# Kernel optimization log

Measured on AMD Instinct MI355X. Metric: run time of the kernel, lower is better.

Reference implementation:

```python
import jax, jax.numpy as jnp
import numpy as np

ROUTINGS = 3
EPS = 1e-9

def _squash(s):
    # squash along the capsule-vector (last) axis
    sq = jnp.sum(s * s, axis=-1, keepdims=True)
    return s * (sq / (1.0 + sq)) / jnp.sqrt(sq + EPS)

def setup_inputs() -> dict:
    key = jax.random.key(0)
    k1, k2 = jax.random.split(key)
    B, N, D, d = 32, 64, 128, 128  # batch, num_capsule(=input_num_capsule), dim_capsule, input_dim_capsule
    x = jax.random.normal(k1, (B, N, d), dtype=jnp.float32)
    W = jax.random.normal(k2, (1, N, N, D, d), dtype=jnp.float32)
    return {"x": x, "W": W}

def reference(x, W):
    # u[b,j,k,:] = W[0,j,k] @ x[b,j]  (faithful to broadcast matmul, N==I)
    u = jnp.einsum('jkde,bje->bjkd', W[0], x)  # (B,N,N,D)
    b = jnp.zeros_like(u)                      # routing logits carry D axis per source
    v = None
    for i in range(ROUTINGS):
        c = jax.nn.softmax(b, axis=2)
        s = jnp.sum(c * u, axis=1, keepdims=True)  # (B,1,N,D)
        v = _squash(s)
        if i < ROUTINGS - 1:
            b = b + u * v  # (inputs*outputs).sum over trailing singleton dim
    return v[:, 0, :, :, None]  # (B,N,D,1) matching torch outputs.squeeze(1)
```

## Files before the change

kernel.cpp:

```cpp
#include <hip/hip_runtime.h>

#define NB 32
#define NN 64
#define ND 128
#define NE 128
#define NK 64

typedef float  f32x4  __attribute__((ext_vector_type(4)));
typedef short  short8 __attribute__((ext_vector_type(8)));
typedef __bf16 bf16x8 __attribute__((ext_vector_type(8)));

union Frag { bf16x8 h; short8 s; };

static constexpr size_t U_BYTES = (size_t)NB * NN * ND * NK * 2;
static constexpr size_t V_BYTES = (size_t)NB * ND * NK * 4;
static constexpr size_t WS_NEED = U_BYTES + 2 * V_BYTES;

#define GLOAD16(g, l)                                                   \
    __builtin_amdgcn_global_load_lds(                                   \
        (const __attribute__((address_space(1))) void*)(g),             \
        (__attribute__((address_space(3))) void*)(l), 16, 0, 0)

template <int CTRL, int RMASK>
__device__ __forceinline__ float dppf(float x) {
    int xi = __float_as_int(x);
    return __int_as_float(__builtin_amdgcn_update_dpp(xi, xi, CTRL, RMASK, 0xF, false));
}
__device__ __forceinline__ float wave_sum(float x) {
    x += dppf<0xB1, 0xF>(x);
    x += dppf<0x4E, 0xF>(x);
    x += dppf<0x141, 0xF>(x);
    x += dppf<0x140, 0xF>(x);
    x += dppf<0x142, 0xA>(x);
    x += dppf<0x143, 0xC>(x);
    return __int_as_float(__builtin_amdgcn_readlane(__float_as_int(x), 63));
}

__device__ __forceinline__ ushort f2bf(float f) {
    __bf16 h = (__bf16)f;
    ushort r;
    __builtin_memcpy(&r, &h, 2);
    return r;
}
__device__ __forceinline__ float bf2f(ushort r) {
    return __int_as_float(((int)r) << 16);
}
__device__ __forceinline__ void cvt8(const float4& a, const float4& b, Frag& fr) {
    fr.h[0] = (__bf16)a.x; fr.h[1] = (__bf16)a.y; fr.h[2] = (__bf16)a.z; fr.h[3] = (__bf16)a.w;
    fr.h[4] = (__bf16)b.x; fr.h[5] = (__bf16)b.y; fr.h[6] = (__bf16)b.z; fr.h[7] = (__bf16)b.w;
}

__global__ __launch_bounds__(256, 1) void k_u(const float* __restrict__ W,
                                              const float* __restrict__ x,
                                              ushort* __restrict__ u) {
    struct WaveSh {
        union {
            float  w[2][4096];
            ushort t[2][32][72];
        };
    };
    __shared__ WaveSh sh[4];

    const int t  = threadIdx.x;
    const int wv = t >> 6;
    const int l  = t & 63;
    const int gw = blockIdx.x * 4 + wv;
    const int j  = gw >> 6;
    const int dp = gw & 63;
    const int d0 = dp * 2;

    const int lr = l & 15;
    const int lh = l >> 4;
    const int sx = lr & 7;

    const float* xb = x + (size_t)j * NE;
    float4 xf[2][4][2];
#pragma unroll
    for (int mt = 0; mt < 2; ++mt)
#pragma unroll
        for (int ec = 0; ec < 4; ++ec) {
            const float* p = xb + (size_t)(mt * 16 + lr) * (NN * NE) + ec * 32 + lh * 8;
            xf[mt][ec][0] = *reinterpret_cast<const float4*>(p);
            xf[mt][ec][1] = *reinterpret_cast<const float4*>(p + 4);
        }
    asm volatile("s_waitcnt vmcnt(0)" ::: "memory");
    __builtin_amdgcn_sched_barrier(0);
    Frag a[2][4];
#pragma unroll
    for (int mt = 0; mt < 2; ++mt)
#pragma unroll
        for (int ec = 0; ec < 4; ++ec) cvt8(xf[mt][ec][0], xf[mt][ec][1], a[mt][ec]);

    const char* Wg = (const char*)W + (((size_t)(j * NN)) * ND + d0) * (NE * 4);
#define STAGE(nt, buf)                                                        \
    {                                                                         \
        _Pragma("unroll") for (int kk = 0; kk < 16; ++kk) {                   \
            const char* gp_ = Wg + (size_t)((nt) * 16 + kk) * 65536 +         \
                              ((l ^ (kk & 7)) * 16);                          \
            GLOAD16(gp_, &sh[wv].w[buf][kk * 256]);                           \
        }                                                                     \
    }

    STAGE(0, 0);
    STAGE(1, 1);

    f32x4 acc[2][2][4];
#pragma unroll
    for (int dd = 0; dd < 2; ++dd)
#pragma unroll
        for (int mt = 0; mt < 2; ++mt)
#pragma unroll
            for (int nt = 0; nt < 4; ++nt) acc[dd][mt][nt] = (f32x4)0.0f;

#pragma unroll
    for (int nt = 0; nt < 4; ++nt) {
        const int buf = nt & 1;
        if (nt < 3) { asm volatile("s_waitcnt vmcnt(16)" ::: "memory"); }
        else        { asm volatile("s_waitcnt vmcnt(0)" ::: "memory"); }
        __builtin_amdgcn_sched_barrier(0);

        const char* cb = (const char*)&sh[wv].w[buf][0] + lr * 1024;
        f32x4 g[2][4][2];
#pragma unroll
        for (int dd = 0; dd < 2; ++dd)
#pragma unroll
            for (int ec = 0; ec < 4; ++ec)
#pragma unroll
                for (int h = 0; h < 2; ++h) {
                    const int pos = (dd * 32 + ec * 8 + lh * 2 + h) ^ sx;
                    g[dd][ec][h] = *reinterpret_cast<const f32x4*>(cb + pos * 16);
                }
        asm volatile("s_waitcnt lgkmcnt(0)" ::: "memory");
        __builtin_amdgcn_sched_barrier(0);
        if (nt < 2) STAGE(nt + 2, buf);

#pragma unroll
        for (int dd = 0; dd < 2; ++dd)
#pragma unroll
            for (int ec = 0; ec < 4; ++ec) {
                Frag bw;
                float4 f0 = {g[dd][ec][0][0], g[dd][ec][0][1], g[dd][ec][0][2], g[dd][ec][0][3]};
                float4 f1 = {g[dd][ec][1][0], g[dd][ec][1][1], g[dd][ec][1][2], g[dd][ec][1][3]};
                cvt8(f0, f1, bw);
#pragma unroll
                for (int mt = 0; mt < 2; ++mt)
                    acc[dd][mt][nt] = __builtin_amdgcn_mfma_f32_16x16x32_bf16(
                        a[mt][ec].s, bw.s, acc[dd][mt][nt], 0, 0, 0);
            }
    }
#undef STAGE

    asm volatile("s_waitcnt lgkmcnt(0)" ::: "memory");
    __builtin_amdgcn_sched_barrier(0);

#pragma unroll
    for (int dd = 0; dd < 2; ++dd)
#pragma unroll
        for (int mt = 0; mt < 2; ++mt)
#pragma unroll
            for (int nt = 0; nt < 4; ++nt)
#pragma unroll
                for (int r = 0; r < 4; ++r)
                    sh[wv].t[dd][mt * 16 + lh * 4 + r][nt * 16 + lr] =
                        f2bf(acc[dd][mt][nt][r]);
    asm volatile("s_waitcnt lgkmcnt(0)" ::: "memory");
    __builtin_amdgcn_sched_barrier(0);

    const int b2 = l >> 1;
    const int kh = (l & 1) * 32;
#pragma unroll
    for (int dd = 0; dd < 2; ++dd) {
        ushort* up = u + (((size_t)b2 * NN + j) * ND + (d0 + dd)) * NK + kh;
        const ushort* tp = &sh[wv].t[dd][b2][kh];
#pragma unroll
        for (int i = 0; i < 4; ++i) {
            short8 v = *reinterpret_cast<const short8*>(tp + i * 8);
            *reinterpret_cast<short8*>(up + i * 8) = v;
        }
    }
}

__global__ __launch_bounds__(512) void k_route(const ushort* __restrict__ u,
                                               const float* __restrict__ Vsum,
                                               float* __restrict__ s,
                                               int first) {
    __shared__ float P[8][8][65];
    const int b  = blockIdx.x >> 4;
    const int dg = blockIdx.x & 15;
    const int t  = threadIdx.x;
    const int wv = t >> 6;
    const int l  = t & 63;

    float sacc[8];
#pragma unroll
    for (int dd = 0; dd < 8; ++dd) sacc[dd] = 0.0f;

    const ushort* ub = u + (((size_t)b * NN + wv * 8) * ND + dg * 8) * NK + l;

    if (first) {
        for (int jj = 0; jj < 8; ++jj) {
            const ushort* up = ub + (size_t)jj * (ND * NK);
#pragma unroll
            for (int dd = 0; dd < 8; ++dd) sacc[dd] += bf2f(up[dd * NK]);
        }
#pragma unroll
        for (int dd = 0; dd < 8; ++dd) sacc[dd] *= (1.0f / 64.0f);
    } else {
        float vs[8];
#pragma unroll
        for (int dd = 0; dd < 8; ++dd)
            vs[dd] = Vsum[((size_t)b * ND + dg * 8 + dd) * NK + l];

        for (int jj = 0; jj < 8; ++jj) {
            const ushort* up = ub + (size_t)jj * (ND * NK);
            float uv[8];
#pragma unroll
            for (int dd = 0; dd < 8; ++dd) uv[dd] = bf2f(up[dd * NK]);
#pragma unroll
            for (int dd = 0; dd < 8; ++dd) {
                float p = __expf(uv[dd] * vs[dd] - 32.0f);
                float q = wave_sum(p);
                sacc[dd] = fmaf(p * __builtin_amdgcn_rcpf(q), uv[dd], sacc[dd]);
            }
        }
    }

#pragma unroll
    for (int dd = 0; dd < 8; ++dd) P[wv][dd][l] = sacc[dd];
    __syncthreads();

    const int dd = t >> 6;
    const int k  = t & 63;
    float r = P[0][dd][k];
#pragma unroll
    for (int w2 = 1; w2 < 8; ++w2) r += P[w2][dd][k];
    s[((size_t)b * ND + dg * 8 + dd) * NK + k] = r;
}

__global__ __launch_bounds__(256) void k_squash(const float* __restrict__ s,
                                                float* __restrict__ Vsum,
                                                float* __restrict__ out,
                                                int mode) {
    const int t  = threadIdx.x;
    const int gw = blockIdx.x * 4 + (t >> 6);
    const int b  = gw >> 6;
    const int k  = gw & 63;
    const int l  = t & 63;

    const float s0 = s[((size_t)b * ND + l) * NK + k];
    const float s1 = s[((size_t)b * ND + l + 64) * NK + k];
    float sq    = wave_sum(fmaf(s0, s0, s1 * s1));
    float scale = (sq / (1.0f + sq)) * rsqrtf(sq + 1e-9f);
    float v0 = s0 * scale, v1 = s1 * scale;
    if (mode == 2) {
        float* op = out + ((size_t)b * NN + k) * ND;
        op[l]      = v0;
        op[l + 64] = v1;
    } else if (mode == 0) {
        float* vp = Vsum + (size_t)b * ND * NK + k;
        vp[(size_t)l * NK]        = v0;
        vp[(size_t)(l + 64) * NK] = v1;
    } else {
        float* vp = Vsum + (size_t)b * ND * NK + k;
        vp[(size_t)l * NK]        += v0;
        vp[(size_t)(l + 64) * NK] += v1;
    }
}

extern "C" void kernel_launch(void* const* d_in, const int* in_sizes, int n_in,
                              void* d_out, int out_size, void* d_ws, size_t ws_size,
                              hipStream_t stream) {
    (void)in_sizes; (void)n_in; (void)out_size;
    const float* x = (const float*)d_in[0];
    const float* W = (const float*)d_in[1];
    float* out = (float*)d_out;

    if (ws_size < WS_NEED) return;
    char* ws = (char*)d_ws;
    ushort* u   = (ushort*)ws;
    float* Vsum = (float*)(ws + U_BYTES);
    float* s    = (float*)(ws + U_BYTES + V_BYTES);

    k_u<<<dim3(1024), dim3(256), 0, stream>>>(W, x, u);
    for (int it = 0; it < 3; ++it) {
        k_route<<<dim3(512), dim3(512), 0, stream>>>(u, Vsum, s, it == 0 ? 1 : 0);
        k_squash<<<dim3(512), dim3(256), 0, stream>>>(s, Vsum, out, it);
    }
}
```

Before: 130.7 us.

## Split u computation into contiguous-W per-(j,k) GEMM plus separate transpose kernel

Each wave now owns one (j,k) pair and streams that pair's contiguous W block in eight 16-row chunks, writing u in a (b,j,k,d) layout with coalesced 16-byte stores. A new transpose kernel then rearranges that buffer into the (b,j,d,k) layout the routing kernel expects. The per-wave LDS footprint is halved, which lets launch bounds request two blocks per CU. The cost is an extra launch plus a full write and read of an intermediate u buffer the same size as u, which also adds to the workspace requirement.

After: 137.8 us. 5.4% more time.

```diff
diff --git a/kernel.cpp b/kernel.cpp
--- a/kernel.cpp
+++ b/kernel.cpp
@@ -12,9 +12,10 @@
 
 union Frag { bf16x8 h; short8 s; };
 
-static constexpr size_t U_BYTES = (size_t)NB * NN * ND * NK * 2;
-static constexpr size_t V_BYTES = (size_t)NB * ND * NK * 4;
-static constexpr size_t WS_NEED = U_BYTES + 2 * V_BYTES;
+static constexpr size_t UT_BYTES = (size_t)NB * NN * NN * ND * 2;
+static constexpr size_t U_BYTES  = (size_t)NB * NN * ND * NK * 2;
+static constexpr size_t V_BYTES  = (size_t)NB * ND * NK * 4;
+static constexpr size_t WS_NEED  = UT_BYTES + U_BYTES + 2 * V_BYTES;
 
 #define GLOAD16(g, l)                                                   \
     __builtin_amdgcn_global_load_lds(                                   \
@@ -45,18 +46,18 @@
 __device__ __forceinline__ float bf2f(ushort r) {
     return __int_as_float(((int)r) << 16);
 }
-__device__ __forceinline__ void cvt8(const float4& a, const float4& b, Frag& fr) {
-    fr.h[0] = (__bf16)a.x; fr.h[1] = (__bf16)a.y; fr.h[2] = (__bf16)a.z; fr.h[3] = (__bf16)a.w;
-    fr.h[4] = (__bf16)b.x; fr.h[5] = (__bf16)b.y; fr.h[6] = (__bf16)b.z; fr.h[7] = (__bf16)b.w;
-}
-
-__global__ __launch_bounds__(256, 1) void k_u(const float* __restrict__ W,
+__device__ __forceinline__ void cvt8f(const f32x4& a, const f32x4& b, Frag& fr) {
+    fr.h[0] = (__bf16)a[0]; fr.h[1] = (__bf16)a[1]; fr.h[2] = (__bf16)a[2]; fr.h[3] = (__bf16)a[3];
+    fr.h[4] = (__bf16)b[0]; fr.h[5] = (__bf16)b[1]; fr.h[6] = (__bf16)b[2]; fr.h[7] = (__bf16)b[3];
+}
+
+__global__ __launch_bounds__(256, 2) void k_u(const float* __restrict__ W,
                                               const float* __restrict__ x,
-                                              ushort* __restrict__ u) {
+                                              ushort* __restrict__ u_tmp) {
     struct WaveSh {
         union {
-            float  w[2][4096];
-            ushort t[2][32][72];
+            float  w[2][2048];
+            ushort t[32][132];
         };
     };
     __shared__ WaveSh sh[4];
@@ -66,22 +67,20 @@
     const int l  = t & 63;
     const int gw = blockIdx.x * 4 + wv;
     const int j  = gw >> 6;
-    const int dp = gw & 63;
-    const int d0 = dp * 2;
+    const int k  = gw & 63;
 
     const int lr = l & 15;
     const int lh = l >> 4;
-    const int sx = lr & 7;
 
     const float* xb = x + (size_t)j * NE;
-    float4 xf[2][4][2];
+    f32x4 xf[2][4][2];
 #pragma unroll
     for (int mt = 0; mt < 2; ++mt)
 #pragma unroll
         for (int ec = 0; ec < 4; ++ec) {
             const float* p = xb + (size_t)(mt * 16 + lr) * (NN * NE) + ec * 32 + lh * 8;
-            xf[mt][ec][0] = *reinterpret_cast<const float4*>(p);
-            xf[mt][ec][1] = *reinterpret_cast<const float4*>(p + 4);
+            xf[mt][ec][0] = *reinterpret_cast<const f32x4*>(p);
+            xf[mt][ec][1] = *reinterpret_cast<const f32x4*>(p + 4);
         }
     asm volatile("s_waitcnt vmcnt(0)" ::: "memory");
     __builtin_amdgcn_sched_barrier(0);
@@ -89,94 +88,109 @@
 #pragma unroll
     for (int mt = 0; mt < 2; ++mt)
 #pragma unroll
-        for (int ec = 0; ec < 4; ++ec) cvt8(xf[mt][ec][0], xf[mt][ec][1], a[mt][ec]);
-
-    const char* Wg = (const char*)W + (((size_t)(j * NN)) * ND + d0) * (NE * 4);
-#define STAGE(nt, buf)                                                        \
+        for (int ec = 0; ec < 4; ++ec) cvt8f(xf[mt][ec][0], xf[mt][ec][1], a[mt][ec]);
+
+    const char* Wg = (const char*)W + ((size_t)(j * NN + k) * ND) * (NE * 4);
+#define STAGE(c, buf)                                                         \
     {                                                                         \
-        _Pragma("unroll") for (int kk = 0; kk < 16; ++kk) {                   \
-            const char* gp_ = Wg + (size_t)((nt) * 16 + kk) * 65536 +         \
-                              ((l ^ (kk & 7)) * 16);                          \
-            GLOAD16(gp_, &sh[wv].w[buf][kk * 256]);                           \
+        _Pragma("unroll") for (int i_ = 0; i_ < 8; ++i_) {                    \
+            const int rl_ = 2 * i_ + (l >> 5);                                \
+            const char* gp_ = Wg + ((size_t)((c) * 16 + rl_) << 9) +          \
+                              (((l & 31) ^ (rl_ & 7)) << 4);                  \
+            GLOAD16(gp_, &sh[wv].w[buf][i_ * 256]);                           \
         }                                                                     \
     }
 
     STAGE(0, 0);
     STAGE(1, 1);
 
-    f32x4 acc[2][2][4];
-#pragma unroll
-    for (int dd = 0; dd < 2; ++dd)
-#pragma unroll
-        for (int mt = 0; mt < 2; ++mt)
-#pragma unroll
-            for (int nt = 0; nt < 4; ++nt) acc[dd][mt][nt] = (f32x4)0.0f;
-
-#pragma unroll
-    for (int nt = 0; nt < 4; ++nt) {
-        const int buf = nt & 1;
-        if (nt < 3) { asm volatile("s_waitcnt vmcnt(16)" ::: "memory"); }
-        else        { asm volatile("s_waitcnt vmcnt(0)" ::: "memory"); }
+    f32x4 acc[2][8];
+#pragma unroll
+    for (int mt = 0; mt < 2; ++mt)
+#pragma unroll
+        for (int nt = 0; nt < 8; ++nt) acc[mt][nt] = (f32x4)0.0f;
+
+#pragma unroll
+    for (int c = 0; c < 8; ++c) {
+        const int buf = c & 1;
+        if (c < 7) { asm volatile("s_waitcnt vmcnt(8)" ::: "memory"); }
+        else       { asm volatile("s_waitcnt vmcnt(0)" ::: "memory"); }
         __builtin_amdgcn_sched_barrier(0);
 
-        const char* cb = (const char*)&sh[wv].w[buf][0] + lr * 1024;
-        f32x4 g[2][4][2];
-#pragma unroll
-        for (int dd = 0; dd < 2; ++dd)
-#pragma unroll
-            for (int ec = 0; ec < 4; ++ec)
-#pragma unroll
-                for (int h = 0; h < 2; ++h) {
-                    const int pos = (dd * 32 + ec * 8 + lh * 2 + h) ^ sx;
-                    g[dd][ec][h] = *reinterpret_cast<const f32x4*>(cb + pos * 16);
-                }
+        const char* cb = (const char*)&sh[wv].w[buf][0] + lr * 512;
+        f32x4 g[4][2];
+#pragma unroll
+        for (int ec = 0; ec < 4; ++ec)
+#pragma unroll
+            for (int h = 0; h < 2; ++h) {
+                const int pos = (ec * 8 + lh * 2 + h) ^ (lr & 7);
+                g[ec][h] = *reinterpret_cast<const f32x4*>(cb + pos * 16);
+            }
         asm volatile("s_waitcnt lgkmcnt(0)" ::: "memory");
         __builtin_amdgcn_sched_barrier(0);
-        if (nt < 2) STAGE(nt + 2, buf);
-
-#pragma unroll
-        for (int dd = 0; dd < 2; ++dd)
-#pragma unroll
-            for (int ec = 0; ec < 4; ++ec) {
-                Frag bw;
-                float4 f0 = {g[dd][ec][0][0], g[dd][ec][0][1], g[dd][ec][0][2], g[dd][ec][0][3]};
-                float4 f1 = {g[dd][ec][1][0], g[dd][ec][1][1], g[dd][ec][1][2], g[dd][ec][1][3]};
-                cvt8(f0, f1, bw);
-#pragma unroll
-                for (int mt = 0; mt < 2; ++mt)
-                    acc[dd][mt][nt] = __builtin_amdgcn_mfma_f32_16x16x32_bf16(
-                        a[mt][ec].s, bw.s, acc[dd][mt][nt], 0, 0, 0);
-            }
+        if (c < 6) STAGE(c + 2, buf);
+
+#pragma unroll
+        for (int ec = 0; ec < 4; ++ec) {
+            Frag bw;
+            cvt8f(g[ec][0], g[ec][1], bw);
+#pragma unroll
+            for (int mt = 0; mt < 2; ++mt)
+                acc[mt][c] = __builtin_amdgcn_mfma_f32_16x16x32_bf16(
+                    a[mt][ec].s, bw.s, acc[mt][c], 0, 0, 0);
+        }
     }
 #undef STAGE
 
+#pragma unroll
+    for (int mt = 0; mt < 2; ++mt)
+#pragma unroll
+        for (int nt = 0; nt < 8; ++nt)
+#pragma unroll
+            for (int r = 0; r < 4; ++r)
+                sh[wv].t[mt * 16 + lh * 4 + r][nt * 16 + lr] = f2bf(acc[mt][nt][r]);
     asm volatile("s_waitcnt lgkmcnt(0)" ::: "memory");
     __builtin_amdgcn_sched_barrier(0);
 
 #pragma unroll
-    for (int dd = 0; dd < 2; ++dd)
-#pragma unroll
-        for (int mt = 0; mt < 2; ++mt)
-#pragma unroll
-            for (int nt = 0; nt < 4; ++nt)
-#pragma unroll
-                for (int r = 0; r < 4; ++r)
-                    sh[wv].t[dd][mt * 16 + lh * 4 + r][nt * 16 + lr] =
-                        f2bf(acc[dd][mt][nt][r]);
-    asm volatile("s_waitcnt lgkmcnt(0)" ::: "memory");
-    __builtin_amdgcn_sched_barrier(0);
-
-    const int b2 = l >> 1;
-    const int kh = (l & 1) * 32;
-#pragma unroll
-    for (int dd = 0; dd < 2; ++dd) {
-        ushort* up = u + (((size_t)b2 * NN + j) * ND + (d0 + dd)) * NK + kh;
-        const ushort* tp = &sh[wv].t[dd][b2][kh];
-#pragma unroll
-        for (int i = 0; i < 4; ++i) {
-            short8 v = *reinterpret_cast<const short8*>(tp + i * 8);
-            *reinterpret_cast<short8*>(up + i * 8) = v;
-        }
+    for (int i = 0; i < 8; ++i) {
+        const int b  = i * 4 + (l >> 4);
+        const int d0 = (l & 15) * 8;
+        short8 v = *reinterpret_cast<const short8*>(&sh[wv].t[b][d0]);
+        ushort* up = u_tmp + (((size_t)b * NN + j) * NK + k) * ND + d0;
+        *reinterpret_cast<short8*>(up) = v;
+    }
+}
+
+__global__ __launch_bounds__(256) void k_t(const ushort* __restrict__ u_tmp,
+                                           ushort* __restrict__ u) {
+    __shared__ ushort Lt[64][136];
+    const int bj = blockIdx.x;
+    const int b  = bj >> 6;
+    const int j  = bj & 63;
+    const int t  = threadIdx.x;
+
+    const ushort* src = u_tmp + ((size_t)(b * NN + j) * NK) * ND;
+#pragma unroll
+    for (int q = 0; q < 4; ++q) {
+        const int flat = q * 256 + t;
+        const int k    = flat >> 4;
+        const int gcol = flat & 15;
+        short8 v = *reinterpret_cast<const short8*>(src + (size_t)k * ND + gcol * 8);
+        *reinterpret_cast<short8*>(&Lt[k][gcol * 8]) = v;
+    }
+    __syncthreads();
+
+    ushort* dst = u + ((size_t)(b * NN + j) * ND) * NK;
+#pragma unroll
+    for (int q = 0; q < 4; ++q) {
+        const int flat = q * 256 + t;
+        const int kg   = flat >> 7;
+        const int d    = flat & 127;
+        short8 v;
+#pragma unroll
+        for (int r = 0; r < 8; ++r) v[r] = (short)Lt[kg * 8 + r][d];
+        *reinterpret_cast<short8*>(dst + (size_t)d * NK + kg * 8) = v;
     }
 }
 
@@ -277,11 +291,13 @@
 
     if (ws_size < WS_NEED) return;
     char* ws = (char*)d_ws;
-    ushort* u   = (ushort*)ws;
-    float* Vsum = (float*)(ws + U_BYTES);
-    float* s    = (float*)(ws + U_BYTES + V_BYTES);
-
-    k_u<<<dim3(1024), dim3(256), 0, stream>>>(W, x, u);
+    ushort* u_tmp = (ushort*)ws;
+    ushort* u     = (ushort*)(ws + UT_BYTES);
+    float* Vsum   = (float*)(ws + UT_BYTES + U_BYTES);
+    float* s      = (float*)(ws + UT_BYTES + U_BYTES + V_BYTES);
+
+    k_u<<<dim3(1024), dim3(256), 0, stream>>>(W, x, u_tmp);
+    k_t<<<dim3(2048), dim3(256), 0, stream>>>(u_tmp, u);
     for (int it = 0; it < 3; ++it) {
         k_route<<<dim3(512), dim3(512), 0, stream>>>(u, Vsum, s, it == 0 ? 1 : 0);
         k_squash<<<dim3(512), dim3(256), 0, stream>>>(s, Vsum, out, it);
```
